# Kernel tuning notes

Measured on AMD Instinct MI355X. Metric: run time of the kernel, lower is better.

Reference implementation:

```python
import jax, jax.numpy as jnp
import numpy as np
import math

NC = 80
TOPK = 10
EPS = 1e-9
DIS = 2.5
BIG = 1e5


def _ciou(b1, b2, eps=EPS):
    # b1: (bs,1,A,4), b2: (bs,G,1,4) -> (bs,G,A)
    b1x1, b1y1, b1x2, b1y2 = b1[..., 0], b1[..., 1], b1[..., 2], b1[..., 3]
    b2x1, b2y1, b2x2, b2y2 = b2[..., 0], b2[..., 1], b2[..., 2], b2[..., 3]
    w1, h1 = b1x2 - b1x1, b1y2 - b1y1 + eps
    w2, h2 = b2x2 - b2x1, b2y2 - b2y1 + eps
    iw = jnp.clip(jnp.minimum(b1x2, b2x2) - jnp.maximum(b1x1, b2x1), 0.0)
    ih = jnp.clip(jnp.minimum(b1y2, b2y2) - jnp.maximum(b1y1, b2y1), 0.0)
    inter = iw * ih
    union = w1 * h1 + w2 * h2 - inter + eps
    iou = inter / union
    cw = jnp.maximum(b1x2, b2x2) - jnp.minimum(b1x1, b2x1)
    ch = jnp.maximum(b1y2, b2y2) - jnp.minimum(b1y1, b2y1)
    c2 = cw * cw + ch * ch + eps
    d2 = ((b2x1 + b2x2 - b1x1 - b1x2) ** 2 + (b2y1 + b2y2 - b1y1 - b1y2) ** 2) / 4.0
    v = (4.0 / math.pi ** 2) * (jnp.arctan(w2 / h2) - jnp.arctan(w1 / h1)) ** 2
    alpha = jax.lax.stop_gradient(v / (v - iou + (1.0 + eps)))
    return iou - (d2 / c2 + v * alpha)


def _cost_matrix(pred_boxes, gt_boxes, mask_gt, pred_scores, gt_labels):
    # geometric candidate masks
    pc = (pred_boxes[..., :2] + pred_boxes[..., 2:]) / 2.0  # (bs,A,2) anchor centers
    pce = pc[:, None, :, :]                                  # (bs,1,A,2)
    in_boxes = jnp.all(pce > gt_boxes[:, :, None, :2], -1) & jnp.all(gt_boxes[:, :, None, 2:] > pce, -1)
    gcen = (gt_boxes[..., :2] + gt_boxes[..., 2:]) / 2.0
    in_centers = jnp.all(pce > (gcen - DIS)[:, :, None, :], -1) & jnp.all((gcen + DIS)[:, :, None, :] > pce, -1)
    both = in_boxes & in_centers                             # (bs,G,A)

    ciou_val = _ciou(pred_boxes[:, None, :, :], gt_boxes[:, :, None, :])  # (bs,G,A)

    # summed BCE over classes against one-hot(gt_label), without (bs,G,A,nc) intermediate:
    # sum_c bce = -sum_c log(1-p_c) - (log p_y - log(1-p_y))
    p = jnp.clip(pred_scores, 1e-7, 1.0 - 1e-7)
    logp = jnp.log(p)
    log1mp = jnp.log1p(-p)
    S = -log1mp.sum(-1)                                      # (bs,A)
    delta = -(logp - log1mp)                                 # (bs,A,nc)
    per_lab = jnp.take_along_axis(jnp.transpose(delta, (0, 2, 1)), gt_labels[:, :, None], axis=1)  # (bs,G,A)
    cls_cost = S[:, None, :] + per_lab

    cost = cls_cost + 3.0 * ciou_val + BIG * (~both).astype(cost_dtype(pred_boxes))
    return cost


def cost_dtype(x):
    return x.dtype


def reference(pred_boxes, gt_boxes, mask_gt, pred_scores, gt_labels):
    cost = _cost_matrix(pred_boxes, gt_boxes, mask_gt, pred_scores, gt_labels)  # (bs,G,A)
    bs, G, A = cost.shape
    # per-GT bottom-k (lowest cost) candidate anchors
    _, idx = jax.lax.top_k(-cost, TOPK)                      # (bs,G,TOPK)
    b_ix = jnp.arange(bs)[:, None, None]
    g_ix = jnp.arange(G)[None, :, None]
    pt_mask = jnp.zeros((bs, G, A), dtype=bool).at[b_ix, g_ix, idx].set(True)
    pt_mask = pt_mask & mask_gt[:, :, None]
    # conflict resolution: anchors claimed by >1 GT go to the min-cost GT
    overlap = pt_mask.sum(1) > 1                             # (bs,A)
    pick = jnp.argmin(jnp.where(pt_mask, cost, jnp.inf), axis=1)  # (bs,A)
    pick_oh = jnp.arange(G)[None, :, None] == pick[:, None, :]    # (bs,G,A)
    final = jnp.where(overlap[:, None, :], pick_oh, pt_mask) & mask_gt[:, :, None]
    return final, cost


def setup_inputs() -> dict:
    key = jax.random.key(0)
    k = jax.random.split(key, 7)
    bs, A, G = 32, 8400, 64
    pc = jax.random.uniform(k[0], (bs, A, 2)) * 640.0
    pwh = jax.random.uniform(k[1], (bs, A, 2)) * 96.0 + 8.0
    pred_boxes = jnp.concatenate([pc - pwh / 2, pc + pwh / 2], -1)
    gc = jax.random.uniform(k[2], (bs, G, 2)) * 640.0
    gwh = jax.random.uniform(k[3], (bs, G, 2)) * 128.0 + 16.0
    gt_boxes = jnp.concatenate([gc - gwh / 2, gc + gwh / 2], -1)
    mask_gt = jax.random.uniform(k[4], (bs, G)) < 0.8
    pred_scores = jax.random.uniform(k[5], (bs, A, NC), minval=1e-4, maxval=1.0 - 1e-4)
    gt_labels = jax.random.randint(k[6], (bs, G), 0, NC, dtype=jnp.int32)
    return {"pred_boxes": pred_boxes, "gt_boxes": gt_boxes, "mask_gt": mask_gt,
            "pred_scores": pred_scores, "gt_labels": gt_labels}
```

## Files before the change

### kernel.cpp

```cpp
#include <hip/hip_runtime.h>
#include <math.h>

#define BS   32
#define A_N  8400
#define G_N  64
#define NC_N 80
#define TK   10
#define DR   48
#define DSTR 65

static __device__ __forceinline__ float fdiv(float n, float d) {
    return n * __builtin_amdgcn_rcpf(d);
}
static __device__ __forceinline__ unsigned sortable(float f) {
    unsigned u = __float_as_uint(f);
    return (u & 0x80000000u) ? ~u : (u | 0x80000000u);
}

__global__ __launch_bounds__(256)
void k_cost(const float* __restrict__ pred_boxes,
            const float* __restrict__ gt_boxes,
            const float* __restrict__ pred_scores,
            const int*   __restrict__ gt_labels,
            float* __restrict__ cost)
{
    __shared__ float4 s_box[G_N];
    __shared__ float4 s_mid[G_N];
    __shared__ float4 s_ctr[G_N];
    __shared__ float4 s_pb[64];
    __shared__ float4 s_pa[64];
    __shared__ float  s_S[4 * 64];
    __shared__ float  s_delta[DR * DSTR];
    __shared__ int    s_lab[G_N], s_ord[G_N], s_rowk[G_N];
    __shared__ int    s_pres[NC_N], s_rank[NC_N];

    const float EPSF = 1e-9f;
    const float LO = 1e-7f;
    const float HI = (float)(1.0 - 1e-7);
    const int t = threadIdx.x;
    const int b = blockIdx.y;

    if (t < G_N) {
        const float4 gb = ((const float4*)gt_boxes)[b * G_N + t];
        s_box[t] = gb;
        const float sx = gb.x + gb.z, sy = gb.y + gb.w;
        const float w2 = gb.z - gb.x, h2 = (gb.w - gb.y) + EPSF;
        s_mid[t] = make_float4(sx, sy, w2 * h2, atanf(w2 / h2));
        const float cx = sx / 2.0f, cy = sy / 2.0f;
        s_ctr[t] = make_float4(cx - 2.5f, cy - 2.5f, cx + 2.5f, cy + 2.5f);
        s_lab[t] = gt_labels[b * G_N + t];
    }
    __syncthreads();
    if (t < G_N) {
        const int myl = s_lab[t];
        int rank = 0;
        for (int j = 0; j < G_N; ++j) {
            const int lj = s_lab[j];
            rank += (lj < myl) || (lj == myl && j < t);
        }
        s_ord[rank] = t;
    }
    if (t < NC_N) {
        int p = 0;
        for (int j = 0; j < G_N; ++j) p |= (s_lab[j] == t);
        s_pres[t] = p;
    }
    __syncthreads();
    if (t < NC_N) {
        int r = 0;
        for (int c = 0; c < t; ++c) r += s_pres[c];
        s_rank[t] = s_pres[t] ? r : -1;
    }
    __syncthreads();
    if (t < G_N) s_rowk[t] = s_rank[s_lab[s_ord[t]]];

    {
        const int q  = t & 3;
        const int al = t >> 2;
        const int a  = blockIdx.x * 64 + al;
        if (a < A_N) {
            const float4* p4 =
                (const float4*)(pred_scores + ((size_t)b * A_N + a) * NC_N + q * 20);
            float4 s0 = p4[0], s1 = p4[1], s2 = p4[2], s3 = p4[3], s4 = p4[4];
            s0.x=fminf(fmaxf(s0.x,LO),HI); s0.y=fminf(fmaxf(s0.y,LO),HI);
            s0.z=fminf(fmaxf(s0.z,LO),HI); s0.w=fminf(fmaxf(s0.w,LO),HI);
            s1.x=fminf(fmaxf(s1.x,LO),HI); s1.y=fminf(fmaxf(s1.y,LO),HI);
            s1.z=fminf(fmaxf(s1.z,LO),HI); s1.w=fminf(fmaxf(s1.w,LO),HI);
            s2.x=fminf(fmaxf(s2.x,LO),HI); s2.y=fminf(fmaxf(s2.y,LO),HI);
            s2.z=fminf(fmaxf(s2.z,LO),HI); s2.w=fminf(fmaxf(s2.w,LO),HI);
            s3.x=fminf(fmaxf(s3.x,LO),HI); s3.y=fminf(fmaxf(s3.y,LO),HI);
            s3.z=fminf(fmaxf(s3.z,LO),HI); s3.w=fminf(fmaxf(s3.w,LO),HI);
            s4.x=fminf(fmaxf(s4.x,LO),HI); s4.y=fminf(fmaxf(s4.y,LO),HI);
            s4.z=fminf(fmaxf(s4.z,LO),HI); s4.w=fminf(fmaxf(s4.w,LO),HI);
            float g1 = (1.0f-s0.x); g1*=(1.0f-s0.y); g1*=(1.0f-s0.z); g1*=(1.0f-s0.w);
            g1*=(1.0f-s1.x); g1*=(1.0f-s1.y); g1*=(1.0f-s1.z); g1*=(1.0f-s1.w);
            float g2 = (1.0f-s2.x); g2*=(1.0f-s2.y); g2*=(1.0f-s2.z); g2*=(1.0f-s2.w);
            g2*=(1.0f-s3.x); g2*=(1.0f-s3.y); g2*=(1.0f-s3.z); g2*=(1.0f-s3.w);
            float g3 = (1.0f-s4.x); g3*=(1.0f-s4.y); g3*=(1.0f-s4.z); g3*=(1.0f-s4.w);
            s_S[q * 64 + al] = (logf(g1) + logf(g2)) + logf(g3);
            const float pv[20] = {s0.x,s0.y,s0.z,s0.w, s1.x,s1.y,s1.z,s1.w,
                                  s2.x,s2.y,s2.z,s2.w, s3.x,s3.y,s3.z,s3.w,
                                  s4.x,s4.y,s4.z,s4.w};
            #pragma unroll
            for (int i = 0; i < 20; ++i) {
                const int r = s_rank[q * 20 + i];
                if (r >= 0 && r < DR)
                    s_delta[r * DSTR + al] =
                        logf((1.0f - pv[i]) * __builtin_amdgcn_rcpf(pv[i]));
            }
            if (q == 0) {
                const float4 pb = ((const float4*)pred_boxes)[(size_t)b * A_N + a];
                s_pb[al] = pb;
                const float pcx = (pb.x + pb.z) / 2.0f;
                const float pcy = (pb.y + pb.w) / 2.0f;
                const float w1  = pb.z - pb.x;
                const float h1  = (pb.w - pb.y) + EPSF;
                s_pa[al] = make_float4(pcx, pcy, w1 * h1, atanf(w1 / h1));
            }
        }
    }
    __syncthreads();

    const int la = t & 63;
    const int gs = t >> 6;
    const int a  = blockIdx.x * 64 + la;
    if (a >= A_N) return;

    const float4 pb = s_pb[la];
    const float4 pa = s_pa[la];
    const float S = -(((s_S[la] + s_S[64 + la]) + s_S[128 + la]) + s_S[192 + la]);
    const float KPI = (float)(4.0 / (M_PI * M_PI));
    const float* prow = pred_scores + ((size_t)b * A_N + a) * NC_N;
    float* crow = cost + (size_t)b * G_N * A_N + a;

    for (int k = gs; k < G_N; k += 4) {
        const int g = s_ord[k];
        const int r = s_rowk[k];
        float delta;
        if (r < DR) {
            delta = s_delta[r * DSTR + la];
        } else {
            const float pc = fminf(fmaxf(prow[s_lab[g]], LO), HI);
            delta = logf((1.0f - pc) * __builtin_amdgcn_rcpf(pc));
        }
        const float Sd = S + delta;
        const float4 gb = s_box[g];
        const float4 gm = s_mid[g];
        const float4 gc = s_ctr[g];
        const float pcx = pa.x, pcy = pa.y, area1 = pa.z, atp = pa.w;

        const bool inb  = (pcx > gb.x) && (pcy > gb.y) && (gb.z > pcx) && (gb.w > pcy);
        const bool inc  = (pcx > gc.x) && (pcy > gc.y) && (gc.z > pcx) && (gc.w > pcy);
        const bool both = inb && inc;

        const float iw    = fmaxf(fminf(pb.z, gb.z) - fmaxf(pb.x, gb.x), 0.0f);
        const float ih    = fmaxf(fminf(pb.w, gb.w) - fmaxf(pb.y, gb.y), 0.0f);
        const float inter = iw * ih;
        const float uni   = ((area1 + gm.z) - inter) + EPSF;
        const float iou   = fdiv(inter, uni);
        const float cw    = fmaxf(pb.z, gb.z) - fminf(pb.x, gb.x);
        const float ch    = fmaxf(pb.w, gb.w) - fminf(pb.y, gb.y);
        const float c2    = ((cw * cw) + (ch * ch)) + EPSF;
        const float dx    = (gm.x - pb.x) - pb.z;
        const float dy    = (gm.y - pb.y) - pb.w;
        const float d2    = ((dx * dx) + (dy * dy)) / 4.0f;
        const float dif   = gm.w - atp;
        const float v     = KPI * (dif * dif);
        const float alpha = fdiv(v, (v - iou) + 1.0f);
        const float ciou  = iou - (fdiv(d2, c2) + v * alpha);

        const float cst   = (Sd + 3.0f * ciou) + (both ? 0.0f : 100000.0f);
        crow[(size_t)g * A_N] = cst;
    }
}

__global__ __launch_bounds__(256)
void k_init(float4* __restrict__ fin, long nf4,
            uint4* __restrict__ slt, long ns4)
{
    const long stride = (long)gridDim.x * 256;
    const float4 z4 = make_float4(0.f, 0.f, 0.f, 0.f);
    const uint4  m4 = make_uint4(~0u, ~0u, ~0u, ~0u);
    for (long i = (long)blockIdx.x * 256 + threadIdx.x; i < nf4; i += stride)
        fin[i] = z4;
    for (long i = (long)blockIdx.x * 256 + threadIdx.x; i < ns4; i += stride)
        slt[i] = m4;
}

__global__ __launch_bounds__(256)
void k_topk(const float* __restrict__ cost, int* __restrict__ topk)
{
    __shared__ unsigned long long s_w[4][TK];

    const int bg   = blockIdx.x;
    const int t    = threadIdx.x;
    const int lane = t & 63;
    const int wid  = t >> 6;
    const float* row = cost + (size_t)bg * A_N;
    const unsigned long long UMAX = ~0ull;

    unsigned long long v[TK];
    #pragma unroll
    for (int j = 0; j < TK; ++j) v[j] = UMAX;

    auto consider = [&](float c, int idx) {
        const unsigned long long key =
            ((unsigned long long)sortable(c) << 14) | (unsigned)idx;
        if (key < v[TK - 1]) {
            v[TK - 1] = key;
            #pragma unroll
            for (int j = TK - 2; j >= 0; --j) {
                const bool sw = v[j + 1] < v[j];
                const unsigned long long tv = v[j];
                v[j]     = sw ? v[j + 1] : v[j];
                v[j + 1] = sw ? tv : v[j + 1];
            }
        }
    };

    const float4* row4 = (const float4*)row;
    const int NV = A_N / 4;
    float4 cur = make_float4(0.f, 0.f, 0.f, 0.f);
    if (t < NV) cur = row4[t];
    for (int i = t; i < NV; i += 256) {
        const int i2 = i + 256;
        float4 nxt = make_float4(0.f, 0.f, 0.f, 0.f);
        if (i2 < NV) nxt = row4[i2];
        const int base = i * 4;
        consider(cur.x, base);
        consider(cur.y, base + 1);
        consider(cur.z, base + 2);
        consider(cur.w, base + 3);
        cur = nxt;
    }

    #pragma unroll
    for (int r = 0; r < TK; ++r) {
        unsigned long long bv = v[0];
        #pragma unroll
        for (int off = 1; off < 64; off <<= 1) {
            const unsigned long long ov = __shfl_xor(bv, off, 64);
            bv = (ov < bv) ? ov : bv;
        }
        if (lane == 0) s_w[wid][r] = bv;
        if (v[0] == bv) {
            #pragma unroll
            for (int j = 0; j < TK - 1; ++j) v[j] = v[j + 1];
            v[TK - 1] = UMAX;
        }
    }
    __syncthreads();

    if (wid == 0) {
        unsigned long long cv = UMAX;
        if (lane < 4 * TK) cv = s_w[lane / TK][lane % TK];
        #pragma unroll
        for (int r = 0; r < TK; ++r) {
            unsigned long long bv = cv;
            #pragma unroll
            for (int off = 1; off < 64; off <<= 1) {
                const unsigned long long ov = __shfl_xor(bv, off, 64);
                bv = (ov < bv) ? ov : bv;
            }
            if (lane == 0) topk[bg * TK + r] = (int)(bv & 16383ull);
            if (cv == bv) cv = UMAX;
        }
    }
}

__global__ __launch_bounds__(256)
void k_scatter1(const float* __restrict__ cost,
                const int*   __restrict__ topk,
                const unsigned char* __restrict__ mask_gt,
                unsigned long long* __restrict__ slot)
{
    const int e = blockIdx.x * 256 + threadIdx.x;
    if (e >= BS * G_N * TK) return;
    const int b = e / (G_N * TK);
    const int r = e % (G_N * TK);
    const int g = r / TK;
    if (!mask_gt[b * G_N + g]) return;
    const int a = topk[e];
    const float c = cost[((size_t)b * G_N + g) * A_N + a];
    const unsigned long long key = ((unsigned long long)sortable(c) << 6) | (unsigned)g;
    atomicMin(&slot[(size_t)b * A_N + a], key);
}

__global__ __launch_bounds__(256)
void k_scatter2(const int* __restrict__ topk,
                const unsigned char* __restrict__ mask_gt,
                const unsigned long long* __restrict__ slot,
                float* __restrict__ final_out)
{
    const int e = blockIdx.x * 256 + threadIdx.x;
    if (e >= BS * G_N * TK) return;
    const int b = e / (G_N * TK);
    const int r = e % (G_N * TK);
    const int g = r / TK;
    if (!mask_gt[b * G_N + g]) return;
    const int a = topk[e];
    if ((int)(slot[(size_t)b * A_N + a] & 63ull) == g)
        final_out[((size_t)b * G_N + g) * A_N + a] = 1.0f;
}

__global__ __launch_bounds__(256)
void k_final(const float* __restrict__ cost,
             const int*   __restrict__ topk,
             const unsigned char* __restrict__ mask_gt,
             float* __restrict__ final_out)
{
    __shared__ int s_top[G_N * TK];
    __shared__ int s_mask[G_N];

    const int t = threadIdx.x;
    const int b = blockIdx.y;
    const int a = blockIdx.x * 256 + t;

    for (int k = t; k < G_N * TK; k += 256) s_top[k] = topk[b * G_N * TK + k];
    if (t < G_N) s_mask[t] = (int)mask_gt[b * G_N + t];
    __syncthreads();
    if (a >= A_N) return;

    unsigned long long member = 0ull;
    int cnt = 0;
    float best = __builtin_inff();
    int bestg = 0;
    for (int g = 0; g < G_N; ++g) {
        bool m = false;
        if (s_mask[g]) {
            #pragma unroll
            for (int j = 0; j < TK; ++j) m = m || (s_top[g * TK + j] == a);
        }
        if (m) {
            member |= (1ull << g);
            ++cnt;
            const float c = cost[((size_t)b * G_N + g) * A_N + a];
            if (c < best) { best = c; bestg = g; }
        }
    }
    const bool ovl = cnt > 1;
    float* frow = final_out + (size_t)b * G_N * A_N + a;
    for (int g = 0; g < G_N; ++g) {
        const bool f = ovl ? (g == bestg) : (((member >> g) & 1ull) != 0ull);
        frow[(size_t)g * A_N] = f ? 1.0f : 0.0f;
    }
}

extern "C" void kernel_launch(void* const* d_in, const int* in_sizes, int n_in,
                              void* d_out, int out_size, void* d_ws, size_t ws_size,
                              hipStream_t stream)
{
    const float* pred_boxes  = (const float*)d_in[0];
    const float* gt_boxes    = (const float*)d_in[1];
    const unsigned char* mask_gt = (const unsigned char*)d_in[2];
    const float* pred_scores = (const float*)d_in[3];
    const int*   gt_labels   = (const int*)d_in[4];

    float* out_final = (float*)d_out;
    float* out_cost  = out_final + (size_t)BS * G_N * A_N;

    const size_t slot_bytes = (size_t)BS * A_N * sizeof(unsigned long long);
    const size_t topk_bytes = (size_t)BS * G_N * TK * sizeof(int);
    unsigned long long* slot = (unsigned long long*)d_ws;
    int* topk_ws = (int*)((char*)d_ws + slot_bytes);
    const bool sparse_ok = ws_size >= slot_bytes + topk_bytes;
    if (!sparse_ok) topk_ws = (int*)d_ws;

    if (sparse_ok) {
        const long nf4 = (long)BS * G_N * A_N / 4;
        const long ns4 = (long)BS * A_N / 2;
        k_init<<<dim3(2048), 256, 0, stream>>>((float4*)out_final, nf4,
                                               (uint4*)slot, ns4);
    }

    k_cost <<<dim3((A_N + 63) / 64, BS), 256, 0, stream>>>(
        pred_boxes, gt_boxes, pred_scores, gt_labels, out_cost);
    k_topk <<<dim3(BS * G_N), 256, 0, stream>>>(out_cost, topk_ws);

    if (sparse_ok) {
        const int NE = BS * G_N * TK;
        k_scatter1<<<dim3((NE + 255) / 256), 256, 0, stream>>>(
            out_cost, topk_ws, mask_gt, slot);
        k_scatter2<<<dim3((NE + 255) / 256), 256, 0, stream>>>(
            topk_ws, mask_gt, slot, out_final);
    } else {
        k_final<<<dim3((A_N + 255) / 256, BS), 256, 0, stream>>>(
            out_cost, topk_ws, mask_gt, out_final);
    }
}
```

Measured before the change: 295.9 us.

## Fuse slot scatter into top-k and write final mask densely from slots

The per-anchor atomicMin slot update moves into the top-k kernel, reusing the sortable cost bits already in the key, so the cost matrix is no longer re-read by a separate scatter kernel. The zero-fill of the final output and the second scatter kernel are replaced by one dense kernel that writes each one-hot column straight from the slot winner. In k_cost, the partial-sum buffer becomes interleaved so it can be read as a float4, and each wave's g loop now walks a contiguous range. In the fallback path, slot and topk share the same workspace, so the new atomics could corrupt the top-k indices.

```diff
diff --git a/kernel.cpp b/kernel.cpp
--- a/kernel.cpp
+++ b/kernel.cpp
@@ -29,7 +29,7 @@
     __shared__ float4 s_ctr[G_N];
     __shared__ float4 s_pb[64];
     __shared__ float4 s_pa[64];
-    __shared__ float  s_S[4 * 64];
+    __shared__ float  s_S[64 * 4];
     __shared__ float  s_delta[DR * DSTR];
     __shared__ int    s_lab[G_N], s_ord[G_N], s_rowk[G_N];
     __shared__ int    s_pres[NC_N], s_rank[NC_N];
@@ -97,7 +97,7 @@
             float g2 = (1.0f-s2.x); g2*=(1.0f-s2.y); g2*=(1.0f-s2.z); g2*=(1.0f-s2.w);
             g2*=(1.0f-s3.x); g2*=(1.0f-s3.y); g2*=(1.0f-s3.z); g2*=(1.0f-s3.w);
             float g3 = (1.0f-s4.x); g3*=(1.0f-s4.y); g3*=(1.0f-s4.z); g3*=(1.0f-s4.w);
-            s_S[q * 64 + al] = (logf(g1) + logf(g2)) + logf(g3);
+            s_S[al * 4 + q] = (logf(g1) + logf(g2)) + logf(g3);
             const float pv[20] = {s0.x,s0.y,s0.z,s0.w, s1.x,s1.y,s1.z,s1.w,
                                   s2.x,s2.y,s2.z,s2.w, s3.x,s3.y,s3.z,s3.w,
                                   s4.x,s4.y,s4.z,s4.w};
@@ -128,12 +128,15 @@
 
     const float4 pb = s_pb[la];
     const float4 pa = s_pa[la];
-    const float S = -(((s_S[la] + s_S[64 + la]) + s_S[128 + la]) + s_S[192 + la]);
+    const float4 Sq = ((const float4*)s_S)[la];
+    const float S = -(((Sq.x + Sq.y) + Sq.z) + Sq.w);
     const float KPI = (float)(4.0 / (M_PI * M_PI));
     const float* prow = pred_scores + ((size_t)b * A_N + a) * NC_N;
     float* crow = cost + (size_t)b * G_N * A_N + a;
-
-    for (int k = gs; k < G_N; k += 4) {
+    const float pcx = pa.x, pcy = pa.y, area1 = pa.z, atp = pa.w;
+
+    #pragma unroll 2
+    for (int k = gs * 16; k < gs * 16 + 16; ++k) {
         const int g = s_ord[k];
         const int r = s_rowk[k];
         float delta;
@@ -147,7 +150,6 @@
         const float4 gb = s_box[g];
         const float4 gm = s_mid[g];
         const float4 gc = s_ctr[g];
-        const float pcx = pa.x, pcy = pa.y, area1 = pa.z, atp = pa.w;
 
         const bool inb  = (pcx > gb.x) && (pcy > gb.y) && (gb.z > pcx) && (gb.w > pcy);
         const bool inc  = (pcx > gc.x) && (pcy > gc.y) && (gc.z > pcx) && (gc.w > pcy);
@@ -175,20 +177,19 @@
 }
 
 __global__ __launch_bounds__(256)
-void k_init(float4* __restrict__ fin, long nf4,
-            uint4* __restrict__ slt, long ns4)
+void k_init(uint4* __restrict__ slt, long ns4)
 {
     const long stride = (long)gridDim.x * 256;
-    const float4 z4 = make_float4(0.f, 0.f, 0.f, 0.f);
-    const uint4  m4 = make_uint4(~0u, ~0u, ~0u, ~0u);
-    for (long i = (long)blockIdx.x * 256 + threadIdx.x; i < nf4; i += stride)
-        fin[i] = z4;
+    const uint4 m4 = make_uint4(~0u, ~0u, ~0u, ~0u);
     for (long i = (long)blockIdx.x * 256 + threadIdx.x; i < ns4; i += stride)
         slt[i] = m4;
 }
 
 __global__ __launch_bounds__(256)
-void k_topk(const float* __restrict__ cost, int* __restrict__ topk)
+void k_topk(const float* __restrict__ cost,
+            const unsigned char* __restrict__ mask_gt,
+            int* __restrict__ topk,
+            unsigned long long* __restrict__ slot)
 {
     __shared__ unsigned long long s_w[4][TK];
 
@@ -252,6 +253,8 @@
     __syncthreads();
 
     if (wid == 0) {
+        const int b = bg >> 6, g = bg & 63;
+        const int msk = (int)mask_gt[bg];
         unsigned long long cv = UMAX;
         if (lane < 4 * TK) cv = s_w[lane / TK][lane % TK];
         #pragma unroll
@@ -262,45 +265,44 @@
                 const unsigned long long ov = __shfl_xor(bv, off, 64);
                 bv = (ov < bv) ? ov : bv;
             }
-            if (lane == 0) topk[bg * TK + r] = (int)(bv & 16383ull);
+            if (lane == 0) {
+                const int a = (int)(bv & 16383ull);
+                topk[bg * TK + r] = a;
+                if (msk) {
+                    const unsigned long long key = ((bv >> 14) << 6) | (unsigned)g;
+                    atomicMin(&slot[(size_t)b * A_N + a], key);
+                }
+            }
             if (cv == bv) cv = UMAX;
         }
     }
 }
 
 __global__ __launch_bounds__(256)
-void k_scatter1(const float* __restrict__ cost,
-                const int*   __restrict__ topk,
-                const unsigned char* __restrict__ mask_gt,
-                unsigned long long* __restrict__ slot)
-{
-    const int e = blockIdx.x * 256 + threadIdx.x;
-    if (e >= BS * G_N * TK) return;
-    const int b = e / (G_N * TK);
-    const int r = e % (G_N * TK);
-    const int g = r / TK;
-    if (!mask_gt[b * G_N + g]) return;
-    const int a = topk[e];
-    const float c = cost[((size_t)b * G_N + g) * A_N + a];
-    const unsigned long long key = ((unsigned long long)sortable(c) << 6) | (unsigned)g;
-    atomicMin(&slot[(size_t)b * A_N + a], key);
-}
-
-__global__ __launch_bounds__(256)
-void k_scatter2(const int* __restrict__ topk,
-                const unsigned char* __restrict__ mask_gt,
-                const unsigned long long* __restrict__ slot,
-                float* __restrict__ final_out)
-{
-    const int e = blockIdx.x * 256 + threadIdx.x;
-    if (e >= BS * G_N * TK) return;
-    const int b = e / (G_N * TK);
-    const int r = e % (G_N * TK);
-    const int g = r / TK;
-    if (!mask_gt[b * G_N + g]) return;
-    const int a = topk[e];
-    if ((int)(slot[(size_t)b * A_N + a] & 63ull) == g)
-        final_out[((size_t)b * G_N + g) * A_N + a] = 1.0f;
+void k_fin(const unsigned long long* __restrict__ slot,
+           float* __restrict__ final_out)
+{
+    const int i = blockIdx.x * 256 + threadIdx.x;
+    const int b = blockIdx.y;
+    if (i >= A_N / 4) return;
+
+    const unsigned long long* sp = slot + (size_t)b * A_N + i * 4;
+    int w0 = -1, w1 = -1, w2 = -1, w3 = -1;
+    {
+        const unsigned long long s0 = sp[0], s1 = sp[1], s2 = sp[2], s3 = sp[3];
+        if (s0 != ~0ull) w0 = (int)(s0 & 63ull);
+        if (s1 != ~0ull) w1 = (int)(s1 & 63ull);
+        if (s2 != ~0ull) w2 = (int)(s2 & 63ull);
+        if (s3 != ~0ull) w3 = (int)(s3 & 63ull);
+    }
+    float4* fp = (float4*)(final_out + (size_t)b * G_N * A_N) + i;
+    for (int g = 0; g < G_N; ++g) {
+        const float4 o = make_float4(w0 == g ? 1.0f : 0.0f,
+                                     w1 == g ? 1.0f : 0.0f,
+                                     w2 == g ? 1.0f : 0.0f,
+                                     w3 == g ? 1.0f : 0.0f);
+        fp[(size_t)g * (A_N / 4)] = o;
+    }
 }
 
 __global__ __launch_bounds__(256)
@@ -367,23 +369,18 @@
     if (!sparse_ok) topk_ws = (int*)d_ws;
 
     if (sparse_ok) {
-        const long nf4 = (long)BS * G_N * A_N / 4;
         const long ns4 = (long)BS * A_N / 2;
-        k_init<<<dim3(2048), 256, 0, stream>>>((float4*)out_final, nf4,
-                                               (uint4*)slot, ns4);
+        k_init<<<dim3(132), 256, 0, stream>>>((uint4*)slot, ns4);
     }
 
     k_cost <<<dim3((A_N + 63) / 64, BS), 256, 0, stream>>>(
         pred_boxes, gt_boxes, pred_scores, gt_labels, out_cost);
-    k_topk <<<dim3(BS * G_N), 256, 0, stream>>>(out_cost, topk_ws);
 
     if (sparse_ok) {
-        const int NE = BS * G_N * TK;
-        k_scatter1<<<dim3((NE + 255) / 256), 256, 0, stream>>>(
-            out_cost, topk_ws, mask_gt, slot);
-        k_scatter2<<<dim3((NE + 255) / 256), 256, 0, stream>>>(
-            topk_ws, mask_gt, slot, out_final);
+        k_topk<<<dim3(BS * G_N), 256, 0, stream>>>(out_cost, mask_gt, topk_ws, slot);
+        k_fin <<<dim3((A_N / 4 + 255) / 256, BS), 256, 0, stream>>>(slot, out_final);
     } else {
+        k_topk<<<dim3(BS * G_N), 256, 0, stream>>>(out_cost, mask_gt, topk_ws, slot);
         k_final<<<dim3((A_N + 255) / 256, BS), 256, 0, stream>>>(
             out_cost, topk_ws, mask_gt, out_final);
     }
```

Result: no change. 299.7 us (+1.3%).
